# Kernel tuning notes

Hardware: AMD Instinct MI355X
Metric: run time of the kernel (lower is better)

The kernel has to match this reference:

```python
import jax, jax.numpy as jnp
import numpy as np

N_NODES = 50000
N_EDGES = 800000
D = 64  # in_dim = hidden_dim = out_dim


def gcn_conv(x, edge_index, W, b, num_nodes):
    """PyG GCNConv: x' = D^{-1/2} (A + I) D^{-1/2} (x W) + b."""
    h = x @ W  # [N, out]
    # add self-loops
    loop = jnp.arange(num_nodes, dtype=edge_index.dtype)
    row = jnp.concatenate([edge_index[0], loop])  # sources j
    col = jnp.concatenate([edge_index[1], loop])  # targets i
    # symmetric normalization
    ones = jnp.ones(row.shape[0], dtype=h.dtype)
    deg = jax.ops.segment_sum(ones, col, num_segments=num_nodes)
    dinv = jnp.where(deg > 0, jax.lax.rsqrt(deg), 0.0)
    norm = dinv[row] * dinv[col]  # [E+N]
    # gather -> scale -> scatter-add
    msg = h[row] * norm[:, None]
    out = jax.ops.segment_sum(msg, col, num_segments=num_nodes)
    return out + b


def setup_inputs() -> dict:
    key = jax.random.key(0)
    k = jax.random.split(key, 6)
    x = jax.random.normal(k[0], (N_NODES, D), dtype=jnp.float32)
    edge_index = jax.random.randint(k[1], (2, N_EDGES), 0, N_NODES, dtype=jnp.int64)
    s = 1.0 / np.sqrt(D)
    W1 = jax.random.uniform(k[2], (D, D), jnp.float32, -s, s)
    b1 = jnp.zeros((D,), jnp.float32)
    W2 = jax.random.uniform(k[3], (D, D), jnp.float32, -s, s)
    b2 = jnp.zeros((D,), jnp.float32)
    return {"x": x, "edge_index": edge_index, "W1": W1, "b1": b1, "W2": W2, "b2": b2}


def reference(x, edge_index, W1, b1, W2, b2):
    h = gcn_conv(x, edge_index, W1, b1, N_NODES)
    h = jax.nn.relu(h)
    out = gcn_conv(h, edge_index, W2, b2, N_NODES)
    return out
```

## Files before the change

kernel.cpp:

```cpp
#include <hip/hip_runtime.h>
#include <hip/hip_fp16.h>

#define N_NODES 50000
#define N_EDGES 800000
#define D 64
#define RANGES 8
#define SLICES 16
#define NPB (N_NODES / RANGES)
#define I4S (N_EDGES / SLICES / 4)
#define CAP 48
#define PFX_BLOCKS (N_NODES / 4)
#define GEMM_BLOCKS (N_NODES / 16)

__global__ __launch_bounds__(1024)
void count_kernel(const int* __restrict__ col, unsigned char* __restrict__ cnt8) {
    __shared__ int cur[NPB];
    int tid = threadIdx.x;
    int r = blockIdx.x & (RANGES - 1), s = blockIdx.x >> 3;
    int lo = r * NPB;
    for (int i = tid; i < NPB; i += 1024) cur[i] = 0;
    __syncthreads();
    const int4* c4 = (const int4*)col;
    for (int i = s * I4S + tid; i < (s + 1) * I4S; i += 1024) {
        int4 c = c4[i];
        int dx = c.x - lo, dy = c.y - lo, dz = c.z - lo, dw = c.w - lo;
        if ((unsigned)dx < NPB) atomicAdd(&cur[dx], 1);
        if ((unsigned)dy < NPB) atomicAdd(&cur[dy], 1);
        if ((unsigned)dz < NPB) atomicAdd(&cur[dz], 1);
        if ((unsigned)dw < NPB) atomicAdd(&cur[dw], 1);
    }
    __syncthreads();
    for (int i = tid; i < NPB; i += 1024)
        cnt8[(size_t)s * N_NODES + lo + i] = (unsigned char)min(cur[i], 255);
}

__device__ __forceinline__ void gemm_body(int blk, const float* __restrict__ X,
                                          const float* __restrict__ W,
                                          __half* __restrict__ H) {
    int tid = threadIdx.x, lane = tid & 63, wv = tid >> 6;
    float w[64];
    #pragma unroll
    for (int k = 0; k < 64; ++k) w[k] = W[k * 64 + lane];
    int node0 = blk * 16 + wv * 4;
    #pragma unroll
    for (int r = 0; r < 4; ++r) {
        int node = node0 + r;
        float xv = X[node * 64 + lane];
        float a0 = 0.f, a1 = 0.f;
        #pragma unroll
        for (int k = 0; k < 64; k += 2) {
            a0 = fmaf(__shfl(xv, k, 64),     w[k],     a0);
            a1 = fmaf(__shfl(xv, k + 1, 64), w[k + 1], a1);
        }
        H[node * 64 + lane] = __float2half(a0 + a1);
    }
}

__global__ __launch_bounds__(256)
void prefix_gemm_kernel(const unsigned char* __restrict__ cnt8,
                        unsigned short* __restrict__ base16,
                        int* __restrict__ cntf, float* __restrict__ dinv,
                        const float* __restrict__ X, const float* __restrict__ W,
                        __half* __restrict__ H) {
    if (blockIdx.x < PFX_BLOCKS) {
        int tid = threadIdx.x, lane = tid & 63;
        int node = blockIdx.x * 4 + (tid >> 6);
        int c = 0;
        if (lane < SLICES) c = cnt8[(size_t)lane * N_NODES + node];
        int pin = c;
        #pragma unroll
        for (int off = 1; off < SLICES; off <<= 1) {
            int t = __shfl_up(pin, off, 64);
            if (lane >= off && lane < SLICES) pin += t;
        }
        if (lane < SLICES)
            base16[(size_t)lane * N_NODES + node] = (unsigned short)(pin - c);
        int n = __shfl(pin, SLICES - 1, 64);
        if (lane == 0) {
            cntf[node] = min(n, CAP);
            dinv[node] = rsqrtf((float)(n + 1));
        }
    } else {
        gemm_body(blockIdx.x - PFX_BLOCKS, X, W, H);
    }
}

__global__ __launch_bounds__(1024)
void place_kernel(const int* __restrict__ row, const int* __restrict__ col,
                  const unsigned short* __restrict__ base16,
                  unsigned short* __restrict__ srcs) {
    __shared__ int cur[NPB];
    int tid = threadIdx.x;
    int r = blockIdx.x & (RANGES - 1), s = blockIdx.x >> 3;
    int lo = r * NPB;
    for (int i = tid; i < NPB; i += 1024)
        cur[i] = base16[(size_t)s * N_NODES + lo + i];
    __syncthreads();
    const int4* c4 = (const int4*)col;
    const int4* r4 = (const int4*)row;
    for (int i = s * I4S + tid; i < (s + 1) * I4S; i += 1024) {
        int4 c  = c4[i];
        int4 rr = r4[i];
        int dx = c.x - lo, dy = c.y - lo, dz = c.z - lo, dw = c.w - lo;
        if ((unsigned)dx < NPB) {
            int p = atomicAdd(&cur[dx], 1);
            if (p < CAP) srcs[(size_t)(lo + dx) * CAP + p] = (unsigned short)rr.x;
        }
        if ((unsigned)dy < NPB) {
            int p = atomicAdd(&cur[dy], 1);
            if (p < CAP) srcs[(size_t)(lo + dy) * CAP + p] = (unsigned short)rr.y;
        }
        if ((unsigned)dz < NPB) {
            int p = atomicAdd(&cur[dz], 1);
            if (p < CAP) srcs[(size_t)(lo + dz) * CAP + p] = (unsigned short)rr.z;
        }
        if ((unsigned)dw < NPB) {
            int p = atomicAdd(&cur[dw], 1);
            if (p < CAP) srcs[(size_t)(lo + dw) * CAP + p] = (unsigned short)rr.w;
        }
    }
}

template<int FUSE>
__global__ __launch_bounds__(256)
void gather_kernel(const __half* __restrict__ H, const int* __restrict__ cnt,
                   const unsigned short* __restrict__ srcs,
                   const float* __restrict__ dinv,
                   const float* __restrict__ bias, const float* __restrict__ W2,
                   void* __restrict__ outp) {
    int tid = threadIdx.x, lane = tid & 63;
    int half = lane >> 5, sub = lane & 31;
    int node = blockIdx.x * 4 + (tid >> 6);
    int n = cnt[node];
    float di = dinv[node];
    const unsigned short* sp = srcs + (size_t)node * CAP;
    int e = 0;
    if (lane < n) {
        int s = sp[lane];
        float w = dinv[s];
        e = s | (((int)__half_as_ushort(__float2half(w))) << 16);
    }
    const __half2* H2 = (const __half2*)H;
    float2 self2 = __half22float2(H2[(size_t)node * 32 + sub]);
    float sw = (half == 0) ? di : 0.f;
    float ax = sw * self2.x, ay = sw * self2.y;
    int i0 = half;
    int nr = (n + 15) & ~15;
    for (int base = 0; base < nr; base += 16) {
        int b0 = base + i0;
        int q0 = __shfl(e, b0 + 0,  64), q1 = __shfl(e, b0 + 2,  64);
        int q2 = __shfl(e, b0 + 4,  64), q3 = __shfl(e, b0 + 6,  64);
        int q4 = __shfl(e, b0 + 8,  64), q5 = __shfl(e, b0 + 10, 64);
        int q6 = __shfl(e, b0 + 12, 64), q7 = __shfl(e, b0 + 14, 64);
        float2 v0 = __half22float2(H2[(size_t)(q0 & 0xFFFF) * 32 + sub]);
        float2 v1 = __half22float2(H2[(size_t)(q1 & 0xFFFF) * 32 + sub]);
        float2 v2 = __half22float2(H2[(size_t)(q2 & 0xFFFF) * 32 + sub]);
        float2 v3 = __half22float2(H2[(size_t)(q3 & 0xFFFF) * 32 + sub]);
        float2 v4 = __half22float2(H2[(size_t)(q4 & 0xFFFF) * 32 + sub]);
        float2 v5 = __half22float2(H2[(size_t)(q5 & 0xFFFF) * 32 + sub]);
        float2 v6 = __half22float2(H2[(size_t)(q6 & 0xFFFF) * 32 + sub]);
        float2 v7 = __half22float2(H2[(size_t)(q7 & 0xFFFF) * 32 + sub]);
        float w0 = __half2float(__ushort_as_half((unsigned short)((unsigned)q0 >> 16)));
        float w1 = __half2float(__ushort_as_half((unsigned short)((unsigned)q1 >> 16)));
        float w2 = __half2float(__ushort_as_half((unsigned short)((unsigned)q2 >> 16)));
        float w3 = __half2float(__ushort_as_half((unsigned short)((unsigned)q3 >> 16)));
        float w4 = __half2float(__ushort_as_half((unsigned short)((unsigned)q4 >> 16)));
        float w5 = __half2float(__ushort_as_half((unsigned short)((unsigned)q5 >> 16)));
        float w6 = __half2float(__ushort_as_half((unsigned short)((unsigned)q6 >> 16)));
        float w7 = __half2float(__ushort_as_half((unsigned short)((unsigned)q7 >> 16)));
        ax = fmaf(w0, v0.x, ax); ay = fmaf(w0, v0.y, ay);
        ax = fmaf(w1, v1.x, ax); ay = fmaf(w1, v1.y, ay);
        ax = fmaf(w2, v2.x, ax); ay = fmaf(w2, v2.y, ay);
        ax = fmaf(w3, v3.x, ax); ay = fmaf(w3, v3.y, ay);
        ax = fmaf(w4, v4.x, ax); ay = fmaf(w4, v4.y, ay);
        ax = fmaf(w5, v5.x, ax); ay = fmaf(w5, v5.y, ay);
        ax = fmaf(w6, v6.x, ax); ay = fmaf(w6, v6.y, ay);
        ax = fmaf(w7, v7.x, ax); ay = fmaf(w7, v7.y, ay);
    }
    ax += __shfl_xor(ax, 32, 64);
    ay += __shfl_xor(ay, 32, 64);
    float cx = __shfl(ax, lane >> 1, 64);
    float cy = __shfl(ay, lane >> 1, 64);
    float sum = (lane & 1) ? cy : cx;
    float gval = di * sum + bias[lane];
    if constexpr (FUSE) {
        gval = fmaxf(gval, 0.f);
        float wc[64];
        #pragma unroll
        for (int k = 0; k < 64; ++k) wc[k] = W2[k * 64 + lane];
        float o0 = 0.f, o1 = 0.f;
        #pragma unroll
        for (int k = 0; k < 64; k += 2) {
            o0 = fmaf(__shfl(gval, k, 64),     wc[k],     o0);
            o1 = fmaf(__shfl(gval, k + 1, 64), wc[k + 1], o1);
        }
        ((__half*)outp)[node * 64 + lane] = __float2half(o0 + o1);
    } else {
        ((float*)outp)[node * 64 + lane] = gval;
    }
}

extern "C" void kernel_launch(void* const* d_in, const int* in_sizes, int n_in,
                              void* d_out, int out_size, void* d_ws, size_t ws_size,
                              hipStream_t stream) {
    const float* x   = (const float*)d_in[0];
    const int*   ei  = (const int*)d_in[1];
    const int*   row = ei;
    const int*   col = ei + N_EDGES;
    const float* W1  = (const float*)d_in[2];
    const float* b1  = (const float*)d_in[3];
    const float* W2  = (const float*)d_in[4];
    const float* b2  = (const float*)d_in[5];
    float* out = (float*)d_out;

    char* p = (char*)d_ws;
    __half* h  = (__half*)p;           p += (size_t)N_NODES * D * 2;
    __half* h2 = (__half*)p;           p += (size_t)N_NODES * D * 2;
    unsigned char*  cnt8   = (unsigned char*)p;  p += (size_t)SLICES * N_NODES;
    unsigned short* base16 = (unsigned short*)p; p += (size_t)SLICES * N_NODES * 2;
    unsigned short* srcs   = (unsigned short*)p; p += (size_t)N_NODES * CAP * 2;
    float* dinv = (float*)p;           p += (size_t)N_NODES * 4;
    int*   cntf = (int*)p;             p += (size_t)N_NODES * 4;

    count_kernel<<<RANGES * SLICES, 1024, 0, stream>>>(col, cnt8);
    prefix_gemm_kernel<<<PFX_BLOCKS + GEMM_BLOCKS, 256, 0, stream>>>(
        cnt8, base16, cntf, dinv, x, W1, h);
    place_kernel<<<RANGES * SLICES, 1024, 0, stream>>>(row, col, base16, srcs);
    gather_kernel<1><<<N_NODES / 4, 256, 0, stream>>>(h, cntf, srcs, dinv, b1, W2, h2);
    gather_kernel<0><<<N_NODES / 4, 256, 0, stream>>>(h2, cntf, srcs, dinv, b2, nullptr, out);
}
```

Baseline: 214.0 us.

## Fuse all GCN stages into one cooperative persistent kernel with split feature halves

Replaces the five separate launches with a single cooperative kernel of 256 blocks × 1024 threads, using grid.sync between the count, prefix+GEMM, place and gather phases. It doubles the edge slices to 32 so the counting and placement work fills all blocks. Features are stored as two 32-wide fp16 halves, and each layer's aggregation runs as two passes of 16 lanes per node, so each pass touches a smaller working set for better L2 reuse. The trade-off is six grid-wide barriers, per-thread register pressure at 1024 threads per block, and lower per-node parallelism in the gathers.

```diff
diff --git a/kernel.cpp b/kernel.cpp
--- a/kernel.cpp
+++ b/kernel.cpp
@@ -1,27 +1,30 @@
 #include <hip/hip_runtime.h>
 #include <hip/hip_fp16.h>
+#include <hip/hip_cooperative_groups.h>
+
+namespace cg = cooperative_groups;
 
 #define N_NODES 50000
 #define N_EDGES 800000
-#define D 64
 #define RANGES 8
-#define SLICES 16
+#define SLICES 32
 #define NPB (N_NODES / RANGES)
 #define I4S (N_EDGES / SLICES / 4)
 #define CAP 48
-#define PFX_BLOCKS (N_NODES / 4)
-#define GEMM_BLOCKS (N_NODES / 16)
-
-__global__ __launch_bounds__(1024)
-void count_kernel(const int* __restrict__ col, unsigned char* __restrict__ cnt8) {
-    __shared__ int cur[NPB];
+#define NBLK 256
+#define NTHR 1024
+#define NWAVE (NBLK * 16)
+#define NODES_PER_BLOCK 196
+
+__device__ __forceinline__ void count_phase(int blk, const int* __restrict__ col,
+                                            unsigned char* __restrict__ cnt8, int* cur) {
     int tid = threadIdx.x;
-    int r = blockIdx.x & (RANGES - 1), s = blockIdx.x >> 3;
+    int r = blk & (RANGES - 1), s = blk >> 3;
     int lo = r * NPB;
-    for (int i = tid; i < NPB; i += 1024) cur[i] = 0;
+    for (int i = tid; i < NPB; i += NTHR) cur[i] = 0;
     __syncthreads();
     const int4* c4 = (const int4*)col;
-    for (int i = s * I4S + tid; i < (s + 1) * I4S; i += 1024) {
+    for (int i = s * I4S + tid; i < (s + 1) * I4S; i += NTHR) {
         int4 c = c4[i];
         int dx = c.x - lo, dy = c.y - lo, dz = c.z - lo, dw = c.w - lo;
         if ((unsigned)dx < NPB) atomicAdd(&cur[dx], 1);
@@ -30,41 +33,19 @@
         if ((unsigned)dw < NPB) atomicAdd(&cur[dw], 1);
     }
     __syncthreads();
-    for (int i = tid; i < NPB; i += 1024)
+    for (int i = tid; i < NPB; i += NTHR)
         cnt8[(size_t)s * N_NODES + lo + i] = (unsigned char)min(cur[i], 255);
 }
 
-__device__ __forceinline__ void gemm_body(int blk, const float* __restrict__ X,
-                                          const float* __restrict__ W,
-                                          __half* __restrict__ H) {
+__device__ __forceinline__ void prefix_gemm_phase(int blk,
+        const unsigned char* __restrict__ cnt8, unsigned short* __restrict__ base16,
+        int* __restrict__ cntf, float* __restrict__ dinv,
+        const float* __restrict__ X, const float* __restrict__ W1,
+        __half* __restrict__ Ha, __half* __restrict__ Hb) {
     int tid = threadIdx.x, lane = tid & 63, wv = tid >> 6;
-    float w[64];
-    #pragma unroll
-    for (int k = 0; k < 64; ++k) w[k] = W[k * 64 + lane];
-    int node0 = blk * 16 + wv * 4;
-    #pragma unroll
-    for (int r = 0; r < 4; ++r) {
-        int node = node0 + r;
-        float xv = X[node * 64 + lane];
-        float a0 = 0.f, a1 = 0.f;
-        #pragma unroll
-        for (int k = 0; k < 64; k += 2) {
-            a0 = fmaf(__shfl(xv, k, 64),     w[k],     a0);
-            a1 = fmaf(__shfl(xv, k + 1, 64), w[k + 1], a1);
-        }
-        H[node * 64 + lane] = __float2half(a0 + a1);
-    }
-}
-
-__global__ __launch_bounds__(256)
-void prefix_gemm_kernel(const unsigned char* __restrict__ cnt8,
-                        unsigned short* __restrict__ base16,
-                        int* __restrict__ cntf, float* __restrict__ dinv,
-                        const float* __restrict__ X, const float* __restrict__ W,
-                        __half* __restrict__ H) {
-    if (blockIdx.x < PFX_BLOCKS) {
-        int tid = threadIdx.x, lane = tid & 63;
-        int node = blockIdx.x * 4 + (tid >> 6);
+    int nb0 = blk * NODES_PER_BLOCK;
+    int nb1 = min(nb0 + NODES_PER_BLOCK, N_NODES);
+    for (int node = nb0 + wv; node < nb1; node += 16) {
         int c = 0;
         if (lane < SLICES) c = cnt8[(size_t)lane * N_NODES + node];
         int pin = c;
@@ -80,25 +61,36 @@
             cntf[node] = min(n, CAP);
             dinv[node] = rsqrtf((float)(n + 1));
         }
-    } else {
-        gemm_body(blockIdx.x - PFX_BLOCKS, X, W, H);
-    }
-}
-
-__global__ __launch_bounds__(1024)
-void place_kernel(const int* __restrict__ row, const int* __restrict__ col,
-                  const unsigned short* __restrict__ base16,
-                  unsigned short* __restrict__ srcs) {
-    __shared__ int cur[NPB];
+    }
+    float w[64];
+    #pragma unroll
+    for (int k = 0; k < 64; ++k) w[k] = W1[k * 64 + lane];
+    for (int node = nb0 + wv; node < nb1; node += 16) {
+        float xv = X[node * 64 + lane];
+        float a0 = 0.f, a1 = 0.f;
+        #pragma unroll
+        for (int k = 0; k < 64; k += 2) {
+            a0 = fmaf(__shfl(xv, k, 64),     w[k],     a0);
+            a1 = fmaf(__shfl(xv, k + 1, 64), w[k + 1], a1);
+        }
+        __half hh = __float2half(a0 + a1);
+        if (lane < 32) Ha[(size_t)node * 32 + lane] = hh;
+        else           Hb[(size_t)node * 32 + lane - 32] = hh;
+    }
+}
+
+__device__ __forceinline__ void place_phase(int blk, const int* __restrict__ row,
+        const int* __restrict__ col, const unsigned short* __restrict__ base16,
+        unsigned short* __restrict__ srcs, int* cur) {
     int tid = threadIdx.x;
-    int r = blockIdx.x & (RANGES - 1), s = blockIdx.x >> 3;
+    int r = blk & (RANGES - 1), s = blk >> 3;
     int lo = r * NPB;
-    for (int i = tid; i < NPB; i += 1024)
+    for (int i = tid; i < NPB; i += NTHR)
         cur[i] = base16[(size_t)s * N_NODES + lo + i];
     __syncthreads();
     const int4* c4 = (const int4*)col;
     const int4* r4 = (const int4*)row;
-    for (int i = s * I4S + tid; i < (s + 1) * I4S; i += 1024) {
+    for (int i = s * I4S + tid; i < (s + 1) * I4S; i += NTHR) {
         int4 c  = c4[i];
         int4 rr = r4[i];
         int dx = c.x - lo, dy = c.y - lo, dz = c.z - lo, dw = c.w - lo;
@@ -121,111 +113,150 @@
     }
 }
 
-template<int FUSE>
-__global__ __launch_bounds__(256)
-void gather_kernel(const __half* __restrict__ H, const int* __restrict__ cnt,
-                   const unsigned short* __restrict__ srcs,
-                   const float* __restrict__ dinv,
-                   const float* __restrict__ bias, const float* __restrict__ W2,
-                   void* __restrict__ outp) {
+template<int MODE>
+__device__ __forceinline__ void gather_pass(int blk,
+        const __half* __restrict__ Hh, const int* __restrict__ cntf,
+        const float* __restrict__ dinv, const unsigned short* __restrict__ srcs,
+        const float* __restrict__ bias, const float* __restrict__ W2,
+        const __half* __restrict__ gAin, __half* __restrict__ o16a,
+        __half* __restrict__ o16b, float* __restrict__ o32) {
     int tid = threadIdx.x, lane = tid & 63;
-    int half = lane >> 5, sub = lane & 31;
-    int node = blockIdx.x * 4 + (tid >> 6);
-    int n = cnt[node];
-    float di = dinv[node];
-    const unsigned short* sp = srcs + (size_t)node * CAP;
-    int e = 0;
-    if (lane < n) {
-        int s = sp[lane];
-        float w = dinv[s];
-        e = s | (((int)__half_as_ushort(__float2half(w))) << 16);
-    }
-    const __half2* H2 = (const __half2*)H;
-    float2 self2 = __half22float2(H2[(size_t)node * 32 + sub]);
-    float sw = (half == 0) ? di : 0.f;
-    float ax = sw * self2.x, ay = sw * self2.y;
-    int i0 = half;
-    int nr = (n + 15) & ~15;
-    for (int base = 0; base < nr; base += 16) {
-        int b0 = base + i0;
-        int q0 = __shfl(e, b0 + 0,  64), q1 = __shfl(e, b0 + 2,  64);
-        int q2 = __shfl(e, b0 + 4,  64), q3 = __shfl(e, b0 + 6,  64);
-        int q4 = __shfl(e, b0 + 8,  64), q5 = __shfl(e, b0 + 10, 64);
-        int q6 = __shfl(e, b0 + 12, 64), q7 = __shfl(e, b0 + 14, 64);
-        float2 v0 = __half22float2(H2[(size_t)(q0 & 0xFFFF) * 32 + sub]);
-        float2 v1 = __half22float2(H2[(size_t)(q1 & 0xFFFF) * 32 + sub]);
-        float2 v2 = __half22float2(H2[(size_t)(q2 & 0xFFFF) * 32 + sub]);
-        float2 v3 = __half22float2(H2[(size_t)(q3 & 0xFFFF) * 32 + sub]);
-        float2 v4 = __half22float2(H2[(size_t)(q4 & 0xFFFF) * 32 + sub]);
-        float2 v5 = __half22float2(H2[(size_t)(q5 & 0xFFFF) * 32 + sub]);
-        float2 v6 = __half22float2(H2[(size_t)(q6 & 0xFFFF) * 32 + sub]);
-        float2 v7 = __half22float2(H2[(size_t)(q7 & 0xFFFF) * 32 + sub]);
-        float w0 = __half2float(__ushort_as_half((unsigned short)((unsigned)q0 >> 16)));
-        float w1 = __half2float(__ushort_as_half((unsigned short)((unsigned)q1 >> 16)));
-        float w2 = __half2float(__ushort_as_half((unsigned short)((unsigned)q2 >> 16)));
-        float w3 = __half2float(__ushort_as_half((unsigned short)((unsigned)q3 >> 16)));
-        float w4 = __half2float(__ushort_as_half((unsigned short)((unsigned)q4 >> 16)));
-        float w5 = __half2float(__ushort_as_half((unsigned short)((unsigned)q5 >> 16)));
-        float w6 = __half2float(__ushort_as_half((unsigned short)((unsigned)q6 >> 16)));
-        float w7 = __half2float(__ushort_as_half((unsigned short)((unsigned)q7 >> 16)));
-        ax = fmaf(w0, v0.x, ax); ay = fmaf(w0, v0.y, ay);
-        ax = fmaf(w1, v1.x, ax); ay = fmaf(w1, v1.y, ay);
-        ax = fmaf(w2, v2.x, ax); ay = fmaf(w2, v2.y, ay);
-        ax = fmaf(w3, v3.x, ax); ay = fmaf(w3, v3.y, ay);
-        ax = fmaf(w4, v4.x, ax); ay = fmaf(w4, v4.y, ay);
-        ax = fmaf(w5, v5.x, ax); ay = fmaf(w5, v5.y, ay);
-        ax = fmaf(w6, v6.x, ax); ay = fmaf(w6, v6.y, ay);
-        ax = fmaf(w7, v7.x, ax); ay = fmaf(w7, v7.y, ay);
-    }
-    ax += __shfl_xor(ax, 32, 64);
-    ay += __shfl_xor(ay, 32, 64);
-    float cx = __shfl(ax, lane >> 1, 64);
-    float cy = __shfl(ay, lane >> 1, 64);
-    float sum = (lane & 1) ? cy : cx;
-    float gval = di * sum + bias[lane];
-    if constexpr (FUSE) {
-        gval = fmaxf(gval, 0.f);
-        float wc[64];
+    int quarter = lane >> 4, sub = lane & 15;
+    int gw = blk * 16 + (tid >> 6);
+    const __half2* H2 = (const __half2*)Hh;
+    float2 bv = ((const float2*)bias)[((MODE == 1 || MODE == 3) ? 16 : 0) + sub];
+    float wc[64];
+    if constexpr (MODE == 1) {
         #pragma unroll
         for (int k = 0; k < 64; ++k) wc[k] = W2[k * 64 + lane];
-        float o0 = 0.f, o1 = 0.f;
-        #pragma unroll
-        for (int k = 0; k < 64; k += 2) {
-            o0 = fmaf(__shfl(gval, k, 64),     wc[k],     o0);
-            o1 = fmaf(__shfl(gval, k + 1, 64), wc[k + 1], o1);
-        }
-        ((__half*)outp)[node * 64 + lane] = __float2half(o0 + o1);
-    } else {
-        ((float*)outp)[node * 64 + lane] = gval;
-    }
+    }
+    for (int node = gw; node < N_NODES; node += NWAVE) {
+        int n = cntf[node];
+        float di = dinv[node];
+        const unsigned short* sp = srcs + (size_t)node * CAP;
+        int e = 0;
+        if (lane < n) {
+            int s = sp[lane];
+            e = s | (((int)__half_as_ushort(__float2half(dinv[s]))) << 16);
+        }
+        float2 self = __half22float2(H2[(size_t)node * 16 + sub]);
+        float sw = (quarter == 0) ? di : 0.f;
+        float ax = sw * self.x, ay = sw * self.y;
+        int nr = (n + 31) & ~31;
+        for (int base = 0; base < nr; base += 32) {
+            int b0 = base + quarter;
+            int q0 = __shfl(e, b0,      64), q1 = __shfl(e, b0 + 4,  64);
+            int q2 = __shfl(e, b0 + 8,  64), q3 = __shfl(e, b0 + 12, 64);
+            int q4 = __shfl(e, b0 + 16, 64), q5 = __shfl(e, b0 + 20, 64);
+            int q6 = __shfl(e, b0 + 24, 64), q7 = __shfl(e, b0 + 28, 64);
+            float2 v0 = __half22float2(H2[(size_t)(q0 & 0xFFFF) * 16 + sub]);
+            float2 v1 = __half22float2(H2[(size_t)(q1 & 0xFFFF) * 16 + sub]);
+            float2 v2 = __half22float2(H2[(size_t)(q2 & 0xFFFF) * 16 + sub]);
+            float2 v3 = __half22float2(H2[(size_t)(q3 & 0xFFFF) * 16 + sub]);
+            float2 v4 = __half22float2(H2[(size_t)(q4 & 0xFFFF) * 16 + sub]);
+            float2 v5 = __half22float2(H2[(size_t)(q5 & 0xFFFF) * 16 + sub]);
+            float2 v6 = __half22float2(H2[(size_t)(q6 & 0xFFFF) * 16 + sub]);
+            float2 v7 = __half22float2(H2[(size_t)(q7 & 0xFFFF) * 16 + sub]);
+            float w0 = __half2float(__ushort_as_half((unsigned short)((unsigned)q0 >> 16)));
+            float w1 = __half2float(__ushort_as_half((unsigned short)((unsigned)q1 >> 16)));
+            float w2 = __half2float(__ushort_as_half((unsigned short)((unsigned)q2 >> 16)));
+            float w3 = __half2float(__ushort_as_half((unsigned short)((unsigned)q3 >> 16)));
+            float w4 = __half2float(__ushort_as_half((unsigned short)((unsigned)q4 >> 16)));
+            float w5 = __half2float(__ushort_as_half((unsigned short)((unsigned)q5 >> 16)));
+            float w6 = __half2float(__ushort_as_half((unsigned short)((unsigned)q6 >> 16)));
+            float w7 = __half2float(__ushort_as_half((unsigned short)((unsigned)q7 >> 16)));
+            ax = fmaf(w0, v0.x, ax); ay = fmaf(w0, v0.y, ay);
+            ax = fmaf(w1, v1.x, ax); ay = fmaf(w1, v1.y, ay);
+            ax = fmaf(w2, v2.x, ax); ay = fmaf(w2, v2.y, ay);
+            ax = fmaf(w3, v3.x, ax); ay = fmaf(w3, v3.y, ay);
+            ax = fmaf(w4, v4.x, ax); ay = fmaf(w4, v4.y, ay);
+            ax = fmaf(w5, v5.x, ax); ay = fmaf(w5, v5.y, ay);
+            ax = fmaf(w6, v6.x, ax); ay = fmaf(w6, v6.y, ay);
+            ax = fmaf(w7, v7.x, ax); ay = fmaf(w7, v7.y, ay);
+        }
+        ax += __shfl_xor(ax, 16, 64); ay += __shfl_xor(ay, 16, 64);
+        ax += __shfl_xor(ax, 32, 64); ay += __shfl_xor(ay, 32, 64);
+        if constexpr (MODE == 0) {
+            float g0 = fmaxf(di * ax + bv.x, 0.f);
+            float g1 = fmaxf(di * ay + bv.y, 0.f);
+            if (lane < 16)
+                ((__half2*)o16a)[(size_t)node * 16 + sub] = __floats2half2_rn(g0, g1);
+        } else if constexpr (MODE == 1) {
+            float g0 = fmaxf(di * ax + bv.x, 0.f);
+            float g1 = fmaxf(di * ay + bv.y, 0.f);
+            int p = max((lane - 32) >> 1, 0);
+            float vx = __shfl(g0, p, 64), vy = __shfl(g1, p, 64);
+            float gv;
+            if (lane < 32) gv = __half2float(gAin[(size_t)node * 32 + lane]);
+            else           gv = (lane & 1) ? vy : vx;
+            float o0 = 0.f, o1 = 0.f;
+            #pragma unroll
+            for (int k = 0; k < 64; k += 2) {
+                o0 = fmaf(__shfl(gv, k, 64),     wc[k],     o0);
+                o1 = fmaf(__shfl(gv, k + 1, 64), wc[k + 1], o1);
+            }
+            __half oh = __float2half(o0 + o1);
+            if (lane < 32) o16a[(size_t)node * 32 + lane] = oh;
+            else           o16b[(size_t)node * 32 + lane - 32] = oh;
+        } else {
+            float r0 = di * ax + bv.x, r1 = di * ay + bv.y;
+            if (lane < 16)
+                ((float2*)o32)[(size_t)node * 32 + (MODE == 3 ? 16 : 0) + sub]
+                    = make_float2(r0, r1);
+        }
+    }
+}
+
+__global__ void __launch_bounds__(NTHR, 4)
+mega(const int* row, const int* col, const float* x, const float* W1,
+     const float* b1, const float* W2, const float* b2, float* out, void* wsraw) {
+    __shared__ int cur[NPB];
+    char* p = (char*)wsraw;
+    __half* Ha  = (__half*)p;           p += (size_t)N_NODES * 32 * 2;
+    __half* Hb  = (__half*)p;           p += (size_t)N_NODES * 32 * 2;
+    __half* gA  = (__half*)p;           p += (size_t)N_NODES * 32 * 2;
+    __half* h2a = (__half*)p;           p += (size_t)N_NODES * 32 * 2;
+    __half* h2b = (__half*)p;           p += (size_t)N_NODES * 32 * 2;
+    unsigned char*  cnt8   = (unsigned char*)p;  p += (size_t)SLICES * N_NODES;
+    unsigned short* base16 = (unsigned short*)p; p += (size_t)SLICES * N_NODES * 2;
+    unsigned short* srcs   = (unsigned short*)p; p += (size_t)N_NODES * CAP * 2;
+    int*   cntf = (int*)p;              p += (size_t)N_NODES * 4;
+    float* dinv = (float*)p;            p += (size_t)N_NODES * 4;
+
+    cg::grid_group grid = cg::this_grid();
+    int blk = blockIdx.x;
+
+    count_phase(blk, col, cnt8, cur);
+    grid.sync();
+    prefix_gemm_phase(blk, cnt8, base16, cntf, dinv, x, W1, Ha, Hb);
+    grid.sync();
+    place_phase(blk, row, col, base16, srcs, cur);
+    grid.sync();
+    gather_pass<0>(blk, Ha, cntf, dinv, srcs, b1, nullptr, nullptr, gA, nullptr, nullptr);
+    grid.sync();
+    gather_pass<1>(blk, Hb, cntf, dinv, srcs, b1, W2, gA, h2a, h2b, nullptr);
+    grid.sync();
+    gather_pass<2>(blk, h2a, cntf, dinv, srcs, b2, nullptr, nullptr, nullptr, nullptr, out);
+    grid.sync();
+    gather_pass<3>(blk, h2b, cntf, dinv, srcs, b2, nullptr, nullptr, nullptr, nullptr, out);
 }
 
 extern "C" void kernel_launch(void* const* d_in, const int* in_sizes, int n_in,
                               void* d_out, int out_size, void* d_ws, size_t ws_size,
                               hipStream_t stream) {
-    const float* x   = (const float*)d_in[0];
     const int*   ei  = (const int*)d_in[1];
     const int*   row = ei;
     const int*   col = ei + N_EDGES;
+    const float* x   = (const float*)d_in[0];
     const float* W1  = (const float*)d_in[2];
     const float* b1  = (const float*)d_in[3];
     const float* W2  = (const float*)d_in[4];
     const float* b2  = (const float*)d_in[5];
     float* out = (float*)d_out;
-
-    char* p = (char*)d_ws;
-    __half* h  = (__half*)p;           p += (size_t)N_NODES * D * 2;
-    __half* h2 = (__half*)p;           p += (size_t)N_NODES * D * 2;
-    unsigned char*  cnt8   = (unsigned char*)p;  p += (size_t)SLICES * N_NODES;
-    unsigned short* base16 = (unsigned short*)p; p += (size_t)SLICES * N_NODES * 2;
-    unsigned short* srcs   = (unsigned short*)p; p += (size_t)N_NODES * CAP * 2;
-    float* dinv = (float*)p;           p += (size_t)N_NODES * 4;
-    int*   cntf = (int*)p;             p += (size_t)N_NODES * 4;
-
-    count_kernel<<<RANGES * SLICES, 1024, 0, stream>>>(col, cnt8);
-    prefix_gemm_kernel<<<PFX_BLOCKS + GEMM_BLOCKS, 256, 0, stream>>>(
-        cnt8, base16, cntf, dinv, x, W1, h);
-    place_kernel<<<RANGES * SLICES, 1024, 0, stream>>>(row, col, base16, srcs);
-    gather_kernel<1><<<N_NODES / 4, 256, 0, stream>>>(h, cntf, srcs, dinv, b1, W2, h2);
-    gather_kernel<0><<<N_NODES / 4, 256, 0, stream>>>(h2, cntf, srcs, dinv, b2, nullptr, out);
-}
+    void*  wsv = d_ws;
+
+    void* args[] = {(void*)&row, (void*)&col, (void*)&x, (void*)&W1,
+                    (void*)&b1, (void*)&W2, (void*)&b2, (void*)&out, (void*)&wsv};
+    hipLaunchCooperativeKernel((const void*)mega, dim3(NBLK), dim3(NTHR),
+                               args, 0, stream);
+}
```

Measured after the change: 452.5 us. 2.11x slower.
